# Optimization experiments

Hardware: AMD Instinct MI355X
Metric: run time of the kernel (lower is better)

Reference implementation:

```python
import jax, jax.numpy as jnp
import numpy as np

N = 100000
E = 1600000
IN_DIM = 128
OUT_DIM = 64


def setup_inputs() -> dict:
    key = jax.random.key(0)
    k_h, k_ei, k_ew, k_W, k_a = jax.random.split(key, 5)
    h = jax.random.normal(k_h, (N, IN_DIM), dtype=jnp.float32)
    edge_index = jax.random.randint(k_ei, (2, E), 0, N, dtype=jnp.int64)
    edge_weight = jax.random.uniform(k_ew, (E,), dtype=jnp.float32)
    # nn.Linear weights (Kaiming-uniform-ish scale)
    W = jax.random.uniform(k_W, (OUT_DIM, IN_DIM), dtype=jnp.float32,
                           minval=-1.0, maxval=1.0) / np.sqrt(IN_DIM)
    a = jax.random.uniform(k_a, (2 * OUT_DIM,), dtype=jnp.float32,
                           minval=-1.0, maxval=1.0) / np.sqrt(2 * OUT_DIM)
    return {"h": h, "edge_index": edge_index, "edge_weight": edge_weight,
            "W": W, "a": a}


def reference(h, edge_index, edge_weight, W, a):
    # Faithful translation of _GATConvSparse.forward (inference; dropout = identity).
    n = h.shape[0]
    src, dst = edge_index[0], edge_index[1]
    Wh = h @ W.T                                  # (N, out_dim)
    d = Wh.shape[1]
    # a(cat([Wh[src], Wh[dst]])) == Wh[src] @ a[:d] + Wh[dst] @ a[d:]
    alpha = Wh[src] @ a[:d] + Wh[dst] @ a[d:]     # (E,)
    alpha = alpha * edge_weight
    # Buggy-but-faithful 'softmax': segment-sum raw scores onto dst nodes...
    alpha_node = jax.ops.segment_sum(alpha, dst, num_segments=n)   # (N,)
    alpha_exp = jnp.exp(alpha_node - alpha_node.max())             # (N,)
    # ...then normalize per-edge exp(src) by sum of exp(src) over each dst segment.
    denom = jax.ops.segment_sum(alpha_exp[src], dst, num_segments=n)  # (N,)
    alpha_norm = alpha_exp[src] / (denom[dst] + 1e-9)              # (E,)
    out = jax.ops.segment_sum(alpha_norm[:, None] * Wh[src], dst,
                              num_segments=n)                      # (N, out_dim)
    return jax.nn.elu(out)
```

## Files before the change

### kernel.cpp

```cpp
#include <hip/hip_runtime.h>
#include <math.h>

#define Nn 100000
#define Ee 1600000
#define IND 128
#define OUTD 64
#define DPB 64
#define NB 1563
#define BSTR 1280
#define CAP 1536
#define GB 1563
#define ECHUNK 4096
#define EB_BLOCKS 391
#define CSCAN_BLOCKS 196
#define AFIX 1048576.0f

using bf16x8 = __attribute__((ext_vector_type(8))) short;
using f32x4 = __attribute__((ext_vector_type(4))) float;

__device__ __forceinline__ unsigned short f2bf(float f) {
    unsigned u = __float_as_uint(f);
    u = u + 0x7FFFu + ((u >> 16) & 1u);
    return (unsigned short)(u >> 16);
}
__device__ __forceinline__ float bf2f(unsigned short h) {
    return __uint_as_float(((unsigned)h) << 16);
}

__device__ __forceinline__ bool probe64(const void* __restrict__ ei) {
    const long long* p = (const long long*)ei;
    bool ok = true;
#pragma unroll
    for (int i = 0; i < 8; ++i) {
        long long v = p[i];
        ok = ok && (v >= 0 && v < Nn);
    }
    return ok;
}

__device__ __forceinline__ void load_edge(const void* ei, int e, bool is64,
                                          int& s, int& d) {
    if (is64) {
        const long long* p = (const long long*)ei;
        s = (int)p[e];
        d = (int)p[Ee + e];
    } else {
        const int* p = (const int*)ei;
        s = p[e];
        d = p[Ee + e];
    }
}

__device__ __forceinline__ int load_dst(const void* ei, int e, bool is64) {
    if (is64) return (int)((const long long*)ei)[Ee + e];
    return ((const int*)ei)[Ee + e];
}

__global__ __launch_bounds__(256) void k_hist(
    const void* __restrict__ ei, unsigned short* __restrict__ counts) {
    __shared__ int cnt[NB];
    int t = threadIdx.x;
    int hc = blockIdx.x;
    for (int i = t; i < NB; i += 256) cnt[i] = 0;
    __syncthreads();
    bool is64 = probe64(ei);
    int base = hc * ECHUNK;
#pragma unroll
    for (int i = 0; i < 16; ++i) {
        int e = base + i * 256 + t;
        if (e < Ee) atomicAdd(&cnt[load_dst(ei, e, is64) >> 6], 1);
    }
    __syncthreads();
    for (int i = t; i < NB; i += 256)
        counts[(size_t)hc * NB + i] = (unsigned short)cnt[i];
}

__global__ __launch_bounds__(512) void k_cscan(
    unsigned short* __restrict__ counts, int* __restrict__ bcnt) {
    int gw = (int)((blockIdx.x * 512 + threadIdx.x) >> 6);
    int lane = threadIdx.x & 63;
    if (gw >= NB) return;
    int run = 0;
    for (int c0 = 0; c0 < EB_BLOCKS; c0 += 64) {
        int c = c0 + lane;
        int v = (c < EB_BLOCKS) ? (int)counts[(size_t)c * NB + gw] : 0;
        int s = v;
#pragma unroll
        for (int d = 1; d < 64; d <<= 1) {
            int u = __shfl_up(s, d, 64);
            if (lane >= d) s += u;
        }
        if (c < EB_BLOCKS)
            counts[(size_t)c * NB + gw] = (unsigned short)(run + s - v);
        run += __shfl(s, 63, 64);
    }
    if (lane == 0) bcnt[gw] = run;
}

__global__ __launch_bounds__(256) void k_gemm(
    const float* __restrict__ h, const float* __restrict__ W,
    const float* __restrict__ a, unsigned short* __restrict__ Whb,
    float* __restrict__ s1, float* __restrict__ s2) {
    __shared__ unsigned short Ash[64][136];
    __shared__ unsigned short Wsh[64][136];
    __shared__ float al[2 * OUTD];
    int bid = blockIdx.x;
    int t = threadIdx.x;

    int R = bid * 64;
    for (int i = t; i < 2048; i += 256) {
        float4 v = ((const float4*)W)[i];
        int r = i >> 5, c = (i & 31) << 2;
        unsigned lo = (unsigned)f2bf(v.x) | ((unsigned)f2bf(v.y) << 16);
        unsigned hi = (unsigned)f2bf(v.z) | ((unsigned)f2bf(v.w) << 16);
        *(uint2*)&Wsh[r][c] = make_uint2(lo, hi);
    }
    if (t < 32) ((float4*)al)[t] = ((const float4*)a)[t];
    for (int i = t; i < 2048; i += 256) {
        int r = i >> 5, c = (i & 31) << 2;
        int n = R + r;
        float4 v = make_float4(0.f, 0.f, 0.f, 0.f);
        if (n < Nn) v = ((const float4*)(h + (size_t)n * IND))[i & 31];
        unsigned lo = (unsigned)f2bf(v.x) | ((unsigned)f2bf(v.y) << 16);
        unsigned hi = (unsigned)f2bf(v.z) | ((unsigned)f2bf(v.w) << 16);
        *(uint2*)&Ash[r][c] = make_uint2(lo, hi);
    }
    __syncthreads();

    int w = t >> 6, l = t & 63;
    int li = l & 15, lg = l >> 4;
    f32x4 acc[4];
#pragma unroll
    for (int nt = 0; nt < 4; ++nt) acc[nt] = (f32x4){0.f, 0.f, 0.f, 0.f};
#pragma unroll
    for (int kk = 0; kk < 4; ++kk) {
        bf16x8 af = *(const bf16x8*)&Ash[w * 16 + li][kk * 32 + lg * 8];
#pragma unroll
        for (int nt = 0; nt < 4; ++nt) {
            bf16x8 bf = *(const bf16x8*)&Wsh[nt * 16 + li][kk * 32 + lg * 8];
            acc[nt] = __builtin_amdgcn_mfma_f32_16x16x32_bf16(af, bf,
                                                              acc[nt],
                                                              0, 0, 0);
        }
    }
    float p1[4] = {0.f, 0.f, 0.f, 0.f};
    float p2[4] = {0.f, 0.f, 0.f, 0.f};
#pragma unroll
    for (int nt = 0; nt < 4; ++nt) {
        float a1v = al[nt * 16 + li];
        float a2v = al[OUTD + nt * 16 + li];
#pragma unroll
        for (int r = 0; r < 4; ++r) {
            float v = acc[nt][r];
            p1[r] += v * a1v;
            p2[r] += v * a2v;
            int row = R + w * 16 + lg * 4 + r;
            if (row < Nn)
                Whb[(size_t)row * OUTD + nt * 16 + li] = f2bf(v);
        }
    }
#pragma unroll
    for (int r = 0; r < 4; ++r) {
#pragma unroll
        for (int m = 1; m < 16; m <<= 1) {
            p1[r] += __shfl_xor(p1[r], m, 64);
            p2[r] += __shfl_xor(p2[r], m, 64);
        }
    }
    if (li < 4) {
        int row = R + w * 16 + lg * 4 + li;
        if (row < Nn) {
            s1[row] = p1[li];
            s2[row] = p2[li];
        }
    }
}

__global__ __launch_bounds__(512) void k_binscatter(
    const void* __restrict__ ei, const float* __restrict__ ew,
    const unsigned short* __restrict__ counts, uint2* __restrict__ bins) {
    __shared__ int cnt[NB];
    __shared__ int gbase[NB];
    __shared__ int lbase[NB];
    __shared__ uint2 srec[ECHUNK];
    __shared__ int saddr[ECHUNK];
    __shared__ int wsum[9];
    int hc = blockIdx.x;
    int t = threadIdx.x;
    for (int i = t; i < NB; i += 512) {
        cnt[i] = 0;
        gbase[i] = (int)counts[(size_t)hc * NB + i];
    }
    __syncthreads();
    bool is64 = probe64(ei);
    int base = hc * ECHUNK;
    unsigned rx[8];
    unsigned rw[8];
    int rb[8];
    int rk[8];
#pragma unroll
    for (int i = 0; i < 8; ++i) {
        int e = base + i * 512 + t;
        rb[i] = -1;
        rx[i] = 0;
        rw[i] = 0;
        rk[i] = 0;
        if (e < Ee) {
            int s, d;
            load_edge(ei, e, is64, s, d);
            rw[i] = __float_as_uint(ew[e]);
            int b = d >> 6;
            rb[i] = b;
            rk[i] = atomicAdd(&cnt[b], 1);
            rx[i] = ((unsigned)s << 7) | ((unsigned)(d & 63) << 24);
        }
    }
    __syncthreads();
    int i0 = t * 4;
    int c0 = (i0 + 0 < NB) ? cnt[i0 + 0] : 0;
    int c1 = (i0 + 1 < NB) ? cnt[i0 + 1] : 0;
    int c2 = (i0 + 2 < NB) ? cnt[i0 + 2] : 0;
    int c3 = (i0 + 3 < NB) ? cnt[i0 + 3] : 0;
    int ts = c0 + c1 + c2 + c3;
    int lane = t & 63;
    int wv = t >> 6;
    int ws = ts;
#pragma unroll
    for (int d = 1; d < 64; d <<= 1) {
        int u = __shfl_up(ws, d, 64);
        if (lane >= d) ws += u;
    }
    if (lane == 63) wsum[wv] = ws;
    __syncthreads();
    if (t == 0) {
        int acc = 0;
#pragma unroll
        for (int j = 0; j < 8; ++j) {
            int v = wsum[j];
            wsum[j] = acc;
            acc += v;
        }
        wsum[8] = acc;
    }
    __syncthreads();
    int tpre = wsum[wv] + (ws - ts);
    if (i0 + 0 < NB) lbase[i0 + 0] = tpre;
    if (i0 + 1 < NB) lbase[i0 + 1] = tpre + c0;
    if (i0 + 2 < NB) lbase[i0 + 2] = tpre + c0 + c1;
    if (i0 + 3 < NB) lbase[i0 + 3] = tpre + c0 + c1 + c2;
    int btot = wsum[8];
    __syncthreads();
#pragma unroll
    for (int i = 0; i < 8; ++i) {
        if (rb[i] >= 0) {
            int slot = lbase[rb[i]] + rk[i];
            srec[slot] = make_uint2(rx[i], rw[i]);
            int off = gbase[rb[i]] + rk[i];
            saddr[slot] = (off < BSTR) ? (rb[i] * BSTR + off) : -1;
        }
    }
    __syncthreads();
    for (int i = t; i < btot; i += 512) {
        int a = saddr[i];
        if (a >= 0) bins[a] = srec[i];
    }
}

__global__ __launch_bounds__(256) void k_balpha(
    const uint2* __restrict__ bins, const int* __restrict__ bcnt,
    const float* __restrict__ s1, const float* __restrict__ s2,
    float* __restrict__ ae) {
    __shared__ int anl[DPB];
    __shared__ int ews[DPB];
    int b = blockIdx.x;
    int t = threadIdx.x;
    if (t < DPB) {
        anl[t] = 0;
        ews[t] = 0;
    }
    __syncthreads();
    int e0 = b * BSTR;
    int c = bcnt[b];
    int e1 = e0 + (c < BSTR ? c : BSTR);
    for (int k = e0 + t; k < e1; k += 256) {
        uint2 r = bins[k];
        int dloc = (int)(r.x >> 24);
        int s = (int)((r.x >> 7) & 0x1FFFF);
        float w = __uint_as_float(r.y);
        atomicAdd(&anl[dloc], (int)rintf(s1[s] * w * AFIX));
        atomicAdd(&ews[dloc], (int)rintf(w * AFIX));
    }
    __syncthreads();
    if (t < DPB) {
        int n = b * DPB + t;
        if (n < Nn) {
            float an = ((float)anl[t] + s2[n] * (float)ews[t]) * (1.f / AFIX);
            ae[n] = expf(an);
        }
    }
}

#define AGG_BODY(NR)                                                         \
    {                                                                        \
        uint2 rr[NR];                                                        \
        unsigned ww[NR];                                                     \
        _Pragma("unroll") for (int j = 0; j < NR; ++j)                       \
            rr[j] = lp[2 * j];                                               \
        _Pragma("unroll") for (int j = 0; j < NR; ++j)                       \
            ww[j] = *(const unsigned*)(whbB + (rr[j].x + hl4));              \
        _Pragma("unroll") for (int j = 0; j < NR; ++j) {                     \
            float aa = __uint_as_float(rr[j].y);                             \
            acc.x += aa * __uint_as_float(ww[j] << 16);                      \
            acc.y += aa * __uint_as_float(ww[j] & 0xFFFF0000u);              \
            den += aa;                                                       \
        }                                                                    \
        lp += 2 * NR;                                                        \
    }

__global__ __launch_bounds__(512, 4) void k_agg(
    const uint2* __restrict__ bins, const int* __restrict__ bcnt,
    const float* __restrict__ ae, const unsigned short* __restrict__ Whb,
    float* __restrict__ out) {
    __shared__ uint2 lrec[CAP];
    __shared__ int cnt[DPB];
    __shared__ int sbase[DPB];
    int b = blockIdx.x;
    int t = threadIdx.x;
    int lane = t & 63;
    int wave = t >> 6;
    int half = lane >> 5;
    int hl = lane & 31;
    unsigned hl4 = (unsigned)hl << 2;
    int e0 = b * BSTR;
    int c = bcnt[b];
    int total = c < BSTR ? c : BSTR;
    int e1 = e0 + total;
    const char* whbB = (const char*)Whb;

    if (t < DPB) cnt[t] = 0;
    __syncthreads();

    unsigned su[CAP / 512];
    float sa[CAP / 512];
    int srk[CAP / 512];
#pragma unroll
    for (int i = 0; i < CAP / 512; ++i) {
        int k = e0 + i * 512 + t;
        srk[i] = -1;
        if (k < e1) {
            uint2 r = bins[k];
            srk[i] = atomicAdd(&cnt[r.x >> 24], 1);
            su[i] = r.x;
            sa[i] = ae[(r.x >> 7) & 0x1FFFF];
        }
    }
    __syncthreads();
    if (t < DPB) {
        int v = cnt[t];
#pragma unroll
        for (int d = 1; d < DPB; d <<= 1) {
            int u = __shfl_up(v, d, 64);
            if (t >= d) v += u;
        }
        sbase[t] = v;
    }
    __syncthreads();
#pragma unroll
    for (int i = 0; i < CAP / 512; ++i) {
        if (srk[i] >= 0) {
            int dloc = su[i] >> 24;
            int pos = sbase[dloc] - cnt[dloc] + srk[i];
            lrec[pos] = make_uint2(su[i] & 0x00FFFF80u,
                                   __float_as_uint(sa[i]));
        }
    }
    __syncthreads();

    for (int d = wave * 8; d < wave * 8 + 8; ++d) {
        int k1 = sbase[d];
        int k = k1 - cnt[d];
        const uint2* lp = lrec + k + half;
        float2 acc = make_float2(0.f, 0.f);
        float den = 0.f;
        for (; k + 15 < k1; k += 16) AGG_BODY(8);
        for (; k + 7 < k1; k += 8) AGG_BODY(4);
        for (; k + 1 < k1; k += 2) AGG_BODY(1);
        if (k < k1) {
            uint2 rA = lrec[k];
            unsigned wA = *(const unsigned*)(whbB + (rA.x + hl4));
            float aA = half ? 0.f : __uint_as_float(rA.y);
            acc.x += aA * __uint_as_float(wA << 16);
            acc.y += aA * __uint_as_float(wA & 0xFFFF0000u);
            den += aA;
        }
        float ax = acc.x + __shfl_xor(acc.x, 32, 64);
        float ay = acc.y + __shfl_xor(acc.y, 32, 64);
        float dn = den + __shfl_xor(den, 32, 64);
        if (half == 0) {
            int n = b * DPB + d;
            if (n < Nn) {
                float inv = 1.f / (dn + 1e-9f);
                float vx = ax * inv;
                float vy = ay * inv;
                vx = vx > 0.f ? vx : expm1f(vx);
                vy = vy > 0.f ? vy : expm1f(vy);
                *(float2*)&out[(size_t)n * OUTD + hl * 2] =
                    make_float2(vx, vy);
            }
        }
    }
}

extern "C" void kernel_launch(void* const* d_in, const int* in_sizes, int n_in,
                              void* d_out, int out_size, void* d_ws,
                              size_t ws_size, hipStream_t stream) {
    const float* h = (const float*)d_in[0];
    const void* ei = d_in[1];
    const float* ew = (const float*)d_in[2];
    const float* W = (const float*)d_in[3];
    const float* a = (const float*)d_in[4];
    float* out = (float*)d_out;

    unsigned short* Whb = (unsigned short*)d_ws;
    float* s1 = (float*)(Whb + (size_t)Nn * OUTD);
    float* s2 = s1 + Nn;
    float* ae = s2 + Nn;
    int* bcnt = (int*)(ae + Nn);
    uint2* bins = (uint2*)(bcnt + 2048);
    unsigned short* counts =
        (unsigned short*)(bins + (size_t)NB * BSTR);

    k_hist<<<EB_BLOCKS, 256, 0, stream>>>(ei, counts);
    k_cscan<<<CSCAN_BLOCKS, 512, 0, stream>>>(counts, bcnt);
    k_gemm<<<GB, 256, 0, stream>>>(h, W, a, Whb, s1, s2);
    k_binscatter<<<EB_BLOCKS, 512, 0, stream>>>(ei, ew, counts, bins);
    k_balpha<<<NB, 256, 0, stream>>>(bins, bcnt, s1, s2, ae);
    k_agg<<<NB, 512, 0, stream>>>(bins, bcnt, ae, Whb, out);
}
```

Baseline: 110.1 us.

## Replace histogram+scan bucketing with two-pass coarse/fine radix scatter via atomics

The per-chunk histogram and column-scan kernels are replaced by a two-level bucketing scheme. Pass 1 scatters edges into 196 coarse destination buckets (512 nodes each), reserving space with global atomics on a cursor. Pass 2 re-sorts each coarse bucket into 8 fine 64-node bins inside shared memory. This removes the 1563-wide counts matrix and its scan traffic, at the cost of writing and reading the edges twice. Edge order within a bin now depends on atomic timing, and overflow is capped by fixed capacities.

```diff
diff --git a/kernel.cpp b/kernel.cpp
--- a/kernel.cpp
+++ b/kernel.cpp
@@ -12,7 +12,8 @@
 #define GB 1563
 #define ECHUNK 4096
 #define EB_BLOCKS 391
-#define CSCAN_BLOCKS 196
+#define NCB 196
+#define CSTR 9216
 #define AFIX 1048576.0f
 
 using bf16x8 = __attribute__((ext_vector_type(8))) short;
@@ -51,146 +52,18 @@
     }
 }
 
-__device__ __forceinline__ int load_dst(const void* ei, int e, bool is64) {
-    if (is64) return (int)((const long long*)ei)[Ee + e];
-    return ((const int*)ei)[Ee + e];
-}
-
-__global__ __launch_bounds__(256) void k_hist(
-    const void* __restrict__ ei, unsigned short* __restrict__ counts) {
-    __shared__ int cnt[NB];
+__global__ __launch_bounds__(512) void k_pass1(
+    const void* __restrict__ ei, const float* __restrict__ ew,
+    int* __restrict__ ccur, uint2* __restrict__ cbins) {
+    __shared__ int cnt[NCB];
+    __shared__ int gbase[NCB];
+    __shared__ int lbase[NCB];
+    __shared__ int btot;
+    __shared__ uint2 srec[ECHUNK];
+    __shared__ int saddr[ECHUNK];
     int t = threadIdx.x;
     int hc = blockIdx.x;
-    for (int i = t; i < NB; i += 256) cnt[i] = 0;
-    __syncthreads();
-    bool is64 = probe64(ei);
-    int base = hc * ECHUNK;
-#pragma unroll
-    for (int i = 0; i < 16; ++i) {
-        int e = base + i * 256 + t;
-        if (e < Ee) atomicAdd(&cnt[load_dst(ei, e, is64) >> 6], 1);
-    }
-    __syncthreads();
-    for (int i = t; i < NB; i += 256)
-        counts[(size_t)hc * NB + i] = (unsigned short)cnt[i];
-}
-
-__global__ __launch_bounds__(512) void k_cscan(
-    unsigned short* __restrict__ counts, int* __restrict__ bcnt) {
-    int gw = (int)((blockIdx.x * 512 + threadIdx.x) >> 6);
-    int lane = threadIdx.x & 63;
-    if (gw >= NB) return;
-    int run = 0;
-    for (int c0 = 0; c0 < EB_BLOCKS; c0 += 64) {
-        int c = c0 + lane;
-        int v = (c < EB_BLOCKS) ? (int)counts[(size_t)c * NB + gw] : 0;
-        int s = v;
-#pragma unroll
-        for (int d = 1; d < 64; d <<= 1) {
-            int u = __shfl_up(s, d, 64);
-            if (lane >= d) s += u;
-        }
-        if (c < EB_BLOCKS)
-            counts[(size_t)c * NB + gw] = (unsigned short)(run + s - v);
-        run += __shfl(s, 63, 64);
-    }
-    if (lane == 0) bcnt[gw] = run;
-}
-
-__global__ __launch_bounds__(256) void k_gemm(
-    const float* __restrict__ h, const float* __restrict__ W,
-    const float* __restrict__ a, unsigned short* __restrict__ Whb,
-    float* __restrict__ s1, float* __restrict__ s2) {
-    __shared__ unsigned short Ash[64][136];
-    __shared__ unsigned short Wsh[64][136];
-    __shared__ float al[2 * OUTD];
-    int bid = blockIdx.x;
-    int t = threadIdx.x;
-
-    int R = bid * 64;
-    for (int i = t; i < 2048; i += 256) {
-        float4 v = ((const float4*)W)[i];
-        int r = i >> 5, c = (i & 31) << 2;
-        unsigned lo = (unsigned)f2bf(v.x) | ((unsigned)f2bf(v.y) << 16);
-        unsigned hi = (unsigned)f2bf(v.z) | ((unsigned)f2bf(v.w) << 16);
-        *(uint2*)&Wsh[r][c] = make_uint2(lo, hi);
-    }
-    if (t < 32) ((float4*)al)[t] = ((const float4*)a)[t];
-    for (int i = t; i < 2048; i += 256) {
-        int r = i >> 5, c = (i & 31) << 2;
-        int n = R + r;
-        float4 v = make_float4(0.f, 0.f, 0.f, 0.f);
-        if (n < Nn) v = ((const float4*)(h + (size_t)n * IND))[i & 31];
-        unsigned lo = (unsigned)f2bf(v.x) | ((unsigned)f2bf(v.y) << 16);
-        unsigned hi = (unsigned)f2bf(v.z) | ((unsigned)f2bf(v.w) << 16);
-        *(uint2*)&Ash[r][c] = make_uint2(lo, hi);
-    }
-    __syncthreads();
-
-    int w = t >> 6, l = t & 63;
-    int li = l & 15, lg = l >> 4;
-    f32x4 acc[4];
-#pragma unroll
-    for (int nt = 0; nt < 4; ++nt) acc[nt] = (f32x4){0.f, 0.f, 0.f, 0.f};
-#pragma unroll
-    for (int kk = 0; kk < 4; ++kk) {
-        bf16x8 af = *(const bf16x8*)&Ash[w * 16 + li][kk * 32 + lg * 8];
-#pragma unroll
-        for (int nt = 0; nt < 4; ++nt) {
-            bf16x8 bf = *(const bf16x8*)&Wsh[nt * 16 + li][kk * 32 + lg * 8];
-            acc[nt] = __builtin_amdgcn_mfma_f32_16x16x32_bf16(af, bf,
-                                                              acc[nt],
-                                                              0, 0, 0);
-        }
-    }
-    float p1[4] = {0.f, 0.f, 0.f, 0.f};
-    float p2[4] = {0.f, 0.f, 0.f, 0.f};
-#pragma unroll
-    for (int nt = 0; nt < 4; ++nt) {
-        float a1v = al[nt * 16 + li];
-        float a2v = al[OUTD + nt * 16 + li];
-#pragma unroll
-        for (int r = 0; r < 4; ++r) {
-            float v = acc[nt][r];
-            p1[r] += v * a1v;
-            p2[r] += v * a2v;
-            int row = R + w * 16 + lg * 4 + r;
-            if (row < Nn)
-                Whb[(size_t)row * OUTD + nt * 16 + li] = f2bf(v);
-        }
-    }
-#pragma unroll
-    for (int r = 0; r < 4; ++r) {
-#pragma unroll
-        for (int m = 1; m < 16; m <<= 1) {
-            p1[r] += __shfl_xor(p1[r], m, 64);
-            p2[r] += __shfl_xor(p2[r], m, 64);
-        }
-    }
-    if (li < 4) {
-        int row = R + w * 16 + lg * 4 + li;
-        if (row < Nn) {
-            s1[row] = p1[li];
-            s2[row] = p2[li];
-        }
-    }
-}
-
-__global__ __launch_bounds__(512) void k_binscatter(
-    const void* __restrict__ ei, const float* __restrict__ ew,
-    const unsigned short* __restrict__ counts, uint2* __restrict__ bins) {
-    __shared__ int cnt[NB];
-    __shared__ int gbase[NB];
-    __shared__ int lbase[NB];
-    __shared__ uint2 srec[ECHUNK];
-    __shared__ int saddr[ECHUNK];
-    __shared__ int wsum[9];
-    int hc = blockIdx.x;
-    int t = threadIdx.x;
-    for (int i = t; i < NB; i += 512) {
-        cnt[i] = 0;
-        gbase[i] = (int)counts[(size_t)hc * NB + i];
-    }
+    for (int i = t; i < NCB; i += 512) cnt[i] = 0;
     __syncthreads();
     bool is64 = probe64(ei);
     int base = hc * ECHUNK;
@@ -209,46 +82,38 @@
             int s, d;
             load_edge(ei, e, is64, s, d);
             rw[i] = __float_as_uint(ew[e]);
-            int b = d >> 6;
-            rb[i] = b;
-            rk[i] = atomicAdd(&cnt[b], 1);
-            rx[i] = ((unsigned)s << 7) | ((unsigned)(d & 63) << 24);
-        }
-    }
-    __syncthreads();
-    int i0 = t * 4;
-    int c0 = (i0 + 0 < NB) ? cnt[i0 + 0] : 0;
-    int c1 = (i0 + 1 < NB) ? cnt[i0 + 1] : 0;
-    int c2 = (i0 + 2 < NB) ? cnt[i0 + 2] : 0;
-    int c3 = (i0 + 3 < NB) ? cnt[i0 + 3] : 0;
-    int ts = c0 + c1 + c2 + c3;
-    int lane = t & 63;
-    int wv = t >> 6;
-    int ws = ts;
-#pragma unroll
-    for (int d = 1; d < 64; d <<= 1) {
-        int u = __shfl_up(ws, d, 64);
-        if (lane >= d) ws += u;
-    }
-    if (lane == 63) wsum[wv] = ws;
-    __syncthreads();
-    if (t == 0) {
-        int acc = 0;
-#pragma unroll
-        for (int j = 0; j < 8; ++j) {
-            int v = wsum[j];
-            wsum[j] = acc;
-            acc += v;
-        }
-        wsum[8] = acc;
-    }
-    __syncthreads();
-    int tpre = wsum[wv] + (ws - ts);
-    if (i0 + 0 < NB) lbase[i0 + 0] = tpre;
-    if (i0 + 1 < NB) lbase[i0 + 1] = tpre + c0;
-    if (i0 + 2 < NB) lbase[i0 + 2] = tpre + c0 + c1;
-    if (i0 + 3 < NB) lbase[i0 + 3] = tpre + c0 + c1 + c2;
-    int btot = wsum[8];
+            int cb = d >> 9;
+            rb[i] = cb;
+            rk[i] = atomicAdd(&cnt[cb], 1);
+            rx[i] = (unsigned)s | ((unsigned)(d & 511) << 17);
+        }
+    }
+    __syncthreads();
+    if (t < 64) {
+        int i0 = t * 4;
+        int c0 = (i0 + 0 < NCB) ? cnt[i0 + 0] : 0;
+        int c1 = (i0 + 1 < NCB) ? cnt[i0 + 1] : 0;
+        int c2 = (i0 + 2 < NCB) ? cnt[i0 + 2] : 0;
+        int c3 = (i0 + 3 < NCB) ? cnt[i0 + 3] : 0;
+        int ts = c0 + c1 + c2 + c3;
+        int sc = ts;
+#pragma unroll
+        for (int d2 = 1; d2 < 64; d2 <<= 1) {
+            int u = __shfl_up(sc, d2, 64);
+            if (t >= d2) sc += u;
+        }
+        int pre = sc - ts;
+        if (i0 + 0 < NCB) lbase[i0 + 0] = pre;
+        if (i0 + 1 < NCB) lbase[i0 + 1] = pre + c0;
+        if (i0 + 2 < NCB) lbase[i0 + 2] = pre + c0 + c1;
+        if (i0 + 3 < NCB) lbase[i0 + 3] = pre + c0 + c1 + c2;
+        if (t == 63) btot = sc;
+    }
+    __syncthreads();
+    for (int i = t; i < NCB; i += 512) {
+        int c = cnt[i];
+        if (c) gbase[i] = atomicAdd(ccur + i, c);
+    }
     __syncthreads();
 #pragma unroll
     for (int i = 0; i < 8; ++i) {
@@ -256,13 +121,167 @@
             int slot = lbase[rb[i]] + rk[i];
             srec[slot] = make_uint2(rx[i], rw[i]);
             int off = gbase[rb[i]] + rk[i];
-            saddr[slot] = (off < BSTR) ? (rb[i] * BSTR + off) : -1;
-        }
-    }
-    __syncthreads();
-    for (int i = t; i < btot; i += 512) {
+            saddr[slot] = (off < CSTR) ? rb[i] * CSTR + off : -1;
+        }
+    }
+    __syncthreads();
+    int bt = btot;
+    for (int i = t; i < bt; i += 512) {
         int a = saddr[i];
-        if (a >= 0) bins[a] = srec[i];
+        if (a >= 0) cbins[a] = srec[i];
+    }
+}
+
+__global__ __launch_bounds__(1024) void k_pass2(
+    const uint2* __restrict__ cbins, const int* __restrict__ ccur,
+    uint2* __restrict__ bins, int* __restrict__ bcnt) {
+    __shared__ int fcur[8];
+    __shared__ int cnt8[8];
+    __shared__ int lb8[8];
+    __shared__ uint2 srec[4096];
+    __shared__ int saddr[4096];
+    int cb = blockIdx.x;
+    int t = threadIdx.x;
+    if (t < 8) fcur[t] = 0;
+    int ctot = ccur[cb];
+    if (ctot > CSTR) ctot = CSTR;
+    const uint2* cbase = cbins + (size_t)cb * CSTR;
+
+    for (int t0 = 0; t0 < ctot; t0 += 4096) {
+        int tilecnt = ctot - t0;
+        if (tilecnt > 4096) tilecnt = 4096;
+        if (t < 8) cnt8[t] = 0;
+        __syncthreads();
+        uint2 rr[4];
+        int rfb[4];
+        int rrk[4];
+#pragma unroll
+        for (int i = 0; i < 4; ++i) {
+            int idx = t0 + i * 1024 + t;
+            rfb[i] = -1;
+            rrk[i] = 0;
+            if (idx < t0 + tilecnt) {
+                uint2 r = cbase[idx];
+                rr[i] = r;
+                int fb = (int)((r.x >> 17) & 0x1FFu) >> 6;
+                rfb[i] = fb;
+                rrk[i] = atomicAdd(&cnt8[fb], 1);
+            }
+        }
+        __syncthreads();
+        if (t == 0) {
+            int acc = 0;
+#pragma unroll
+            for (int j = 0; j < 8; ++j) {
+                lb8[j] = acc;
+                acc += cnt8[j];
+            }
+        }
+        __syncthreads();
+#pragma unroll
+        for (int i = 0; i < 4; ++i) {
+            if (rfb[i] >= 0) {
+                int slot = lb8[rfb[i]] + rrk[i];
+                unsigned x = rr[i].x;
+                unsigned s = x & 0x1FFFFu;
+                unsigned dl = (x >> 17) & 0x1FFu;
+                srec[slot] = make_uint2((s << 7) | ((dl & 63u) << 24),
+                                        rr[i].y);
+                int off = fcur[rfb[i]] + rrk[i];
+                int fine = cb * 8 + rfb[i];
+                saddr[slot] = (off < BSTR) ? fine * BSTR + off : -1;
+            }
+        }
+        __syncthreads();
+        if (t < 8) fcur[t] += cnt8[t];
+        for (int i = t; i < tilecnt; i += 1024) {
+            int a = saddr[i];
+            if (a >= 0) bins[a] = srec[i];
+        }
+        __syncthreads();
+    }
+    if (t < 8) {
+        int fine = cb * 8 + t;
+        if (fine < NB) bcnt[fine] = fcur[t] < BSTR ? fcur[t] : BSTR;
+    }
+}
+
+__global__ __launch_bounds__(256) void k_gemm(
+    const float* __restrict__ h, const float* __restrict__ W,
+    const float* __restrict__ a, unsigned short* __restrict__ Whb,
+    float* __restrict__ s1, float* __restrict__ s2) {
+    __shared__ unsigned short Ash[64][136];
+    __shared__ unsigned short Wsh[64][136];
+    __shared__ float al[2 * OUTD];
+    int bid = blockIdx.x;
+    int t = threadIdx.x;
+
+    int R = bid * 64;
+    for (int i = t; i < 2048; i += 256) {
+        float4 v = ((const float4*)W)[i];
+        int r = i >> 5, c = (i & 31) << 2;
+        unsigned lo = (unsigned)f2bf(v.x) | ((unsigned)f2bf(v.y) << 16);
+        unsigned hi = (unsigned)f2bf(v.z) | ((unsigned)f2bf(v.w) << 16);
+        *(uint2*)&Wsh[r][c] = make_uint2(lo, hi);
+    }
+    if (t < 32) ((float4*)al)[t] = ((const float4*)a)[t];
+    for (int i = t; i < 2048; i += 256) {
+        int r = i >> 5, c = (i & 31) << 2;
+        int n = R + r;
+        float4 v = make_float4(0.f, 0.f, 0.f, 0.f);
+        if (n < Nn) v = ((const float4*)(h + (size_t)n * IND))[i & 31];
+        unsigned lo = (unsigned)f2bf(v.x) | ((unsigned)f2bf(v.y) << 16);
+        unsigned hi = (unsigned)f2bf(v.z) | ((unsigned)f2bf(v.w) << 16);
+        *(uint2*)&Ash[r][c] = make_uint2(lo, hi);
+    }
+    __syncthreads();
+
+    int w = t >> 6, l = t & 63;
+    int li = l & 15, lg = l >> 4;
+    f32x4 acc[4];
+#pragma unroll
+    for (int nt = 0; nt < 4; ++nt) acc[nt] = (f32x4){0.f, 0.f, 0.f, 0.f};
+#pragma unroll
+    for (int kk = 0; kk < 4; ++kk) {
+        bf16x8 af = *(const bf16x8*)&Ash[w * 16 + li][kk * 32 + lg * 8];
+#pragma unroll
+        for (int nt = 0; nt < 4; ++nt) {
+            bf16x8 bf = *(const bf16x8*)&Wsh[nt * 16 + li][kk * 32 + lg * 8];
+            acc[nt] = __builtin_amdgcn_mfma_f32_16x16x32_bf16(af, bf,
+                                                              acc[nt],
+                                                              0, 0, 0);
+        }
+    }
+    float p1[4] = {0.f, 0.f, 0.f, 0.f};
+    float p2[4] = {0.f, 0.f, 0.f, 0.f};
+#pragma unroll
+    for (int nt = 0; nt < 4; ++nt) {
+        float a1v = al[nt * 16 + li];
+        float a2v = al[OUTD + nt * 16 + li];
+#pragma unroll
+        for (int r = 0; r < 4; ++r) {
+            float v = acc[nt][r];
+            p1[r] += v * a1v;
+            p2[r] += v * a2v;
+            int row = R + w * 16 + lg * 4 + r;
+            if (row < Nn)
+                Whb[(size_t)row * OUTD + nt * 16 + li] = f2bf(v);
+        }
+    }
+#pragma unroll
+    for (int r = 0; r < 4; ++r) {
+#pragma unroll
+        for (int m = 1; m < 16; m <<= 1) {
+            p1[r] += __shfl_xor(p1[r], m, 64);
+            p2[r] += __shfl_xor(p2[r], m, 64);
+        }
+    }
+    if (li < 4) {
+        int row = R + w * 16 + lg * 4 + li;
+        if (row < Nn) {
+            s1[row] = p1[li];
+            s2[row] = p2[li];
+        }
     }
 }
 
@@ -426,14 +445,15 @@
     float* s2 = s1 + Nn;
     float* ae = s2 + Nn;
     int* bcnt = (int*)(ae + Nn);
-    uint2* bins = (uint2*)(bcnt + 2048);
-    unsigned short* counts =
-        (unsigned short*)(bins + (size_t)NB * BSTR);
-
-    k_hist<<<EB_BLOCKS, 256, 0, stream>>>(ei, counts);
-    k_cscan<<<CSCAN_BLOCKS, 512, 0, stream>>>(counts, bcnt);
+    int* ccur = bcnt + 2048;
+    uint2* bins = (uint2*)(ccur + 256);
+    uint2* cbins = bins + (size_t)NB * BSTR;
+
+    hipMemsetAsync(ccur, 0, 256 * sizeof(int), stream);
+
     k_gemm<<<GB, 256, 0, stream>>>(h, W, a, Whb, s1, s2);
-    k_binscatter<<<EB_BLOCKS, 512, 0, stream>>>(ei, ew, counts, bins);
+    k_pass1<<<EB_BLOCKS, 512, 0, stream>>>(ei, ew, ccur, cbins);
+    k_pass2<<<NCB, 1024, 0, stream>>>(cbins, ccur, bins, bcnt);
     k_balpha<<<NB, 256, 0, stream>>>(bins, bcnt, s1, s2, ae);
     k_agg<<<NB, 512, 0, stream>>>(bins, bcnt, ae, Whb, out);
 }
```

Result: no change. 108.8 us (-1.2%).
